# Performance work log

Hardware: AMD Instinct MI355X
Metric: run time of the kernel (lower is better)

The kernel has to match this reference:

```python
import jax, jax.numpy as jnp
import numpy as np

B, N, C, C_OUT, LAYERS, ORDER = 512, 207, 207, 512, 2, 2
EPS = 1e-5


def setup_inputs() -> dict:
    key = jax.random.key(0)
    ks = jax.random.split(key, 12)
    C3 = (ORDER * 1 + 1) * C  # support_len=1 (adaptive only), order=2 -> 3*C
    inp = {
        "x": jax.random.normal(ks[0], (B, N, C), dtype=jnp.float32),
        "nodevec1": jax.random.normal(ks[1], (N, 10), dtype=jnp.float32),
        "nodevec2": jax.random.normal(ks[2], (10, N), dtype=jnp.float32),
        # per-layer gcn 1x1 conv: (layers, C_out=C, C_in=3C) + bias
        "Wg": jax.random.normal(ks[3], (LAYERS, C, C3), dtype=jnp.float32) * (1.0 / np.sqrt(C3)),
        "bg": jax.random.normal(ks[4], (LAYERS, C), dtype=jnp.float32) * 0.01,
        # per-layer BatchNorm1d (eval mode) params over channel dim C
        "gamma": 1.0 + 0.1 * jax.random.normal(ks[5], (LAYERS, C), dtype=jnp.float32),
        "beta": 0.1 * jax.random.normal(ks[6], (LAYERS, C), dtype=jnp.float32),
        "rmean": 0.1 * jax.random.normal(ks[7], (LAYERS, C), dtype=jnp.float32),
        "rvar": jax.random.uniform(ks[8], (LAYERS, C), dtype=jnp.float32, minval=0.5, maxval=1.5),
        # final Conv1d(C, C_OUT, k=1)
        "Wm": jax.random.normal(ks[9], (C_OUT, C), dtype=jnp.float32) * (1.0 / np.sqrt(C)),
        "bm": jax.random.normal(ks[10], (C_OUT,), dtype=jnp.float32) * 0.01,
    }
    return inp


def reference(x, nodevec1, nodevec2, Wg, bg, gamma, beta, rmean, rvar, Wm, bm):
    # x: (B, N, C) -> (B, C, N)
    h = jnp.transpose(x, (0, 2, 1))
    # adaptive adjacency: softmax(relu(E1 @ E2), axis=1), shape (N, N)
    adp = jax.nn.softmax(jax.nn.relu(nodevec1 @ nodevec2), axis=1)
    for i in range(LAYERS):
        # diffusion conv: out[b,c,w] = sum_v h[b,c,v] * A[w,v]  (einsum 'ncvl,nwv->ncwl')
        x1 = jnp.einsum('bcv,wv->bcw', h, adp)
        x2 = jnp.einsum('bcv,wv->bcw', x1, adp)
        cat = jnp.concatenate([h, x1, x2], axis=1)  # (B, 3C, N)
        # 1x1 conv (linear over channels) + bias
        g = jnp.einsum('bcn,oc->bon', cat, Wg[i]) + bg[i][None, :, None]
        # BatchNorm1d in eval mode (dropout is identity at inference)
        inv = gamma[i] / jnp.sqrt(rvar[i] + EPS)
        h = g * inv[None, :, None] + (beta[i] - rmean[i] * inv)[None, :, None]
    # final Conv1d 1x1: C -> C_OUT
    out = jnp.einsum('bcn,oc->bon', h, Wm) + bm[None, :, None]  # (B, C_OUT, N)
    return jnp.transpose(out, (0, 2, 1))  # (B, N, C_OUT)
```

## Files before the change

kernel.cpp:

```cpp
#include <hip/hip_runtime.h>
#include <hip/hip_bf16.h>

#define B 512
#define N 207
#define C 207
#define CO 512
#define NLAYERS 2
#define EPS 1e-5f

#define STRIDE 224
#define ROWS 208
#define KSTEPS 7
#define RS ((size_t)ROWS*STRIDE)
#define XSTR 232

typedef unsigned short ushort;
typedef short s8v __attribute__((ext_vector_type(8)));
typedef float f4 __attribute__((ext_vector_type(4)));
typedef unsigned short u16x4 __attribute__((ext_vector_type(4)));

__device__ __forceinline__ ushort f2bu(float f) {
    __hip_bfloat16 h = __float2bfloat16(f);
    return __builtin_bit_cast(ushort, h);
}
__device__ __forceinline__ float bu2f(ushort u) {
    union { unsigned int u; float f; } v; v.u = ((unsigned int)u) << 16;
    return v.f;
}
__device__ __forceinline__ u16x4 packbf4(f4 v) {
    u16x4 r;
    #pragma unroll
    for (int i = 0; i < 4; ++i) r[i] = f2bu(v[i]);
    return r;
}

__global__ void adp_kernel(const float* __restrict__ nv1, const float* __restrict__ nv2,
                           ushort* __restrict__ P1) {
    int w = blockIdx.x, j = threadIdx.x;
    __shared__ float red[256];
    if (w >= 207) {
        if (j < STRIDE) P1[w*STRIDE + j] = 0;
        return;
    }
    float val = 0.f;
    if (j < 207) {
        float acc = 0.f;
        #pragma unroll
        for (int k = 0; k < 10; ++k) acc += nv1[w*10 + k] * nv2[k*207 + j];
        val = fmaxf(acc, 0.f);
    }
    red[j] = (j < 207) ? val : -1e30f;
    __syncthreads();
    for (int off = 128; off > 0; off >>= 1) {
        if (j < off) red[j] = fmaxf(red[j], red[j+off]);
        __syncthreads();
    }
    float m = red[0];
    __syncthreads();
    float e = (j < 207) ? expf(val - m) : 0.f;
    red[j] = e;
    __syncthreads();
    for (int off = 128; off > 0; off >>= 1) {
        if (j < off) red[j] += red[j+off];
        __syncthreads();
    }
    float inv = 1.f / red[0];
    if (j < STRIDE) P1[w*STRIDE + j] = f2bu(e * inv);
}

__global__ void p2_kernel(const ushort* __restrict__ P1, ushort* __restrict__ P2) {
    int v = blockIdx.x*16 + threadIdx.x;
    int w = blockIdx.y*16 + threadIdx.y;
    if (w < STRIDE && v < STRIDE) {
        float acc = 0.f;
        for (int u = 0; u < 207; ++u) acc += bu2f(P1[w*STRIDE + u]) * bu2f(P1[u*STRIDE + v]);
        P2[w*STRIDE + v] = f2bu(acc);
    }
}

__global__ void bn_kernel(const float* __restrict__ gamma, const float* __restrict__ beta,
                          const float* __restrict__ rmean, const float* __restrict__ rvar,
                          const float* __restrict__ bg,
                          float* __restrict__ binv, float* __restrict__ bfold) {
    int i = blockIdx.x*256 + threadIdx.x;
    if (i >= NLAYERS*ROWS) return;
    int l = i / ROWS, o = i % ROWS;
    float iv = 0.f, bf = 0.f;
    if (o < 207) {
        float g = gamma[l*207 + o];
        iv = g * rsqrtf(rvar[l*207 + o] + EPS);
        bf = bg[l*207 + o]*iv + beta[l*207 + o] - rmean[l*207 + o]*iv;
    }
    binv[i] = iv; bfold[i] = bf;
}

__global__ void wg_prep(const float* __restrict__ Wg, ushort* __restrict__ Wgp) {
    int idx = blockIdx.x*256 + threadIdx.x;
    if (idx >= NLAYERS*3*ROWS*STRIDE) return;
    int k = idx % STRIDE;
    int o = (idx / STRIDE) % ROWS;
    int seg = (idx / (STRIDE*ROWS)) % 3;
    int l = idx / (STRIDE*ROWS*3);
    float v = (o < 207 && k < 207) ? Wg[((size_t)(l*207 + o))*621 + seg*207 + k] : 0.f;
    Wgp[idx] = f2bu(v);
}

__global__ void wm_prep(const float* __restrict__ Wm, ushort* __restrict__ Wmp) {
    int idx = blockIdx.x*256 + threadIdx.x;
    if (idx >= CO*STRIDE) return;
    int k = idx % STRIDE, o = idx / STRIDE;
    Wmp[idx] = f2bu(k < 207 ? Wm[o*207 + k] : 0.f);
}

__global__ void h0_kernel(const float* __restrict__ x, ushort* __restrict__ Hcv,
                          ushort* __restrict__ Hnc) {
    __shared__ float t[32][33];
    int b = blockIdx.z;
    int n0 = blockIdx.x*32, c0 = blockIdx.y*32;
    int tx = threadIdx.x, ty = threadIdx.y;
    for (int i = ty; i < 32; i += 8) {
        int n = n0 + i, c = c0 + tx;
        t[i][tx] = (n < 207 && c < 207) ? x[((size_t)b*207 + n)*207 + c] : 0.f;
    }
    __syncthreads();
    size_t base = (size_t)b*RS;
    for (int i = ty; i < 32; i += 8) {
        int n = n0 + i, c = c0 + tx;
        if (n < ROWS && c < STRIDE) Hnc[base + (size_t)n*STRIDE + c] = f2bu(t[i][tx]);
    }
    for (int i = ty; i < 32; i += 8) {
        int c = c0 + i, n = n0 + tx;
        if (c < ROWS && n < STRIDE) Hcv[base + (size_t)c*STRIDE + n] = f2bu(t[tx][i]);
    }
}

template<int ROUNDS_>
__device__ __forceinline__ void stage512(ushort* __restrict__ tile,
                                         const ushort* __restrict__ src,
                                         int rbase, int rmax, int kbase, int tid) {
    int lane = tid & 63, wave = tid >> 6;
    #pragma unroll
    for (int i = 0; i < ROUNDS_; ++i) {
        int r = rbase + i*128 + wave*16 + (lane >> 2);
        r = (r > rmax) ? rmax : r;
        const ushort* g = src + (size_t)r*STRIDE + kbase + (lane & 3)*8;
        ushort* l = tile + i*4096 + wave*512;
        __builtin_amdgcn_global_load_lds(
            (const __attribute__((address_space(1))) void*)g,
            (__attribute__((address_space(3))) void*)l, 16, 0, 0);
    }
}

#define WAIT_VM(n) asm volatile("s_waitcnt vmcnt(" #n ")" ::: "memory")
#define WAIT_LGKM0 asm volatile("s_waitcnt lgkmcnt(0)" ::: "memory")

__global__ __launch_bounds__(512, 2)
void layer_kernel(const ushort* __restrict__ Hcv, const ushort* __restrict__ Hnc,
                  const ushort* __restrict__ P1, const ushort* __restrict__ P2,
                  const ushort* __restrict__ Wgl,
                  const float* __restrict__ bi, const float* __restrict__ bsh,
                  ushort* __restrict__ Hcv_out, ushort* __restrict__ Hnc_out) {
    __shared__ __align__(16) ushort lds[75776];
    ushort* A1t = lds;
    ushort* A2t = lds + 12288;
    ushort* Bt  = lds + 24576;
    ushort* Wgt = lds + 59392;
    ushort* X1l = lds;
    ushort* X2l = lds + 29696;
    ushort* Hnct = lds;

    int tile = blockIdx.x;
    int b = blockIdx.y;
    int n0 = tile*128;
    size_t boff = (size_t)b*RS;
    const ushort* Hcvb = Hcv + boff;
    const ushort* Hncb = Hnc + boff;

    int tid = threadIdx.x, lane = tid & 63, wid = tid >> 6;
    int frow = lane & 15, fko = (lane >> 4)*8, g4 = (lane >> 4)*4;

    int wmA = wid >> 1, wnA = wid & 1;
    f4 aX1[2][8], aX2[2][8];
    #pragma unroll
    for (int i = 0; i < 2; ++i)
        #pragma unroll
        for (int j = 0; j < 8; ++j) { aX1[i][j] = (f4)0.f; aX2[i][j] = (f4)0.f; }

    #pragma unroll
    for (int t = 0; t < 2; ++t) {
        stage512<1>(A1t + t*4096, P1, n0, 223, t*32, tid);
        stage512<1>(A2t + t*4096, P2, n0, 223, t*32, tid);
        stage512<2>(Bt  + t*8192, Hcvb, 0, 207, t*32, tid);
    }

    for (int ks = 0; ks < KSTEPS; ++ks) {
        int bi3 = ks % 3;
        if (ks <= 4) {
            int t = ks + 2, b3 = t % 3;
            stage512<1>(A1t + b3*4096, P1, n0, 223, t*32, tid);
            stage512<1>(A2t + b3*4096, P2, n0, 223, t*32, tid);
            stage512<2>(Bt  + b3*8192, Hcvb, 0, 207, t*32, tid);
            WAIT_VM(8);
        } else if (ks == 5) {
            stage512<2>(Wgt, Wgl + RS, 0, 207, 0, tid);
            WAIT_VM(6);
        } else {
            WAIT_VM(2);
        }
        __builtin_amdgcn_s_barrier();
        s8v a1[2], a2[2], bfr[8];
        #pragma unroll
        for (int f = 0; f < 2; ++f) {
            a1[f] = *(const s8v*)&A1t[bi3*4096 + (wmA*32 + f*16 + frow)*32 + fko];
            a2[f] = *(const s8v*)&A2t[bi3*4096 + (wmA*32 + f*16 + frow)*32 + fko];
        }
        #pragma unroll
        for (int f = 0; f < 8; ++f)
            bfr[f] = *(const s8v*)&Bt[bi3*8192 + (wnA*128 + f*16 + frow)*32 + fko];
        #pragma unroll
        for (int fm = 0; fm < 2; ++fm)
            #pragma unroll
            for (int fn = 0; fn < 8; ++fn) {
                aX1[fm][fn] = __builtin_amdgcn_mfma_f32_16x16x32_bf16(bfr[fn], a1[fm], aX1[fm][fn], 0, 0, 0);
                aX2[fm][fn] = __builtin_amdgcn_mfma_f32_16x16x32_bf16(bfr[fn], a2[fm], aX2[fm][fn], 0, 0, 0);
            }
        WAIT_LGKM0;
        __builtin_amdgcn_s_barrier();
    }
    #pragma unroll
    for (int fm = 0; fm < 2; ++fm) {
        int w = wmA*32 + fm*16 + (lane & 15);
        #pragma unroll
        for (int fn = 0; fn < 8; ++fn) {
            int cq = wnA*128 + fn*16 + g4;
            if (cq < STRIDE) {
                *(u16x4*)&X1l[w*XSTR + cq] = packbf4(aX1[fm][fn]);
                *(u16x4*)&X2l[w*XSTR + cq] = packbf4(aX2[fm][fn]);
            }
        }
    }
    WAIT_LGKM0;
    __builtin_amdgcn_s_barrier();

    int wmB = wid >> 1, wnB = wid & 1;
    f4 aG[4][4];
    #pragma unroll
    for (int i = 0; i < 4; ++i)
        #pragma unroll
        for (int j = 0; j < 4; ++j) aG[i][j] = (f4)0.f;

    const int NK = 3*KSTEPS;
    for (int ks = 0; ks < NK; ++ks) {
        int cur = ks & 1;
        int seg = (ks < 7) ? 1 : (ks < 14) ? 2 : 0;
        int k0 = (ks % 7)*32;
        if (ks + 1 < NK) {
            int ks1 = ks + 1;
            int seg1v = (ks1 < 7) ? 1 : (ks1 < 14) ? 2 : 0;
            int kk1 = (ks1 % 7)*32;
            stage512<2>(Wgt + (cur^1)*8192, Wgl + (size_t)seg1v*RS, 0, 207, kk1, tid);
        }
        if (ks >= 7 && ks <= 13) {
            stage512<1>(Hnct + (ks-7)*4096, Hncb, n0, 207, (ks-7)*32, tid);
        }
        if (ks == NK-1) { WAIT_VM(0); }
        else if (ks >= 7 && ks <= 13) { WAIT_VM(3); }
        else { WAIT_VM(2); }
        __builtin_amdgcn_s_barrier();
        s8v a[4], bfr[4];
        #pragma unroll
        for (int f = 0; f < 4; ++f)
            a[f] = *(const s8v*)&Wgt[cur*8192 + (wmB*64 + f*16 + frow)*32 + fko];
        if (seg == 0) {
            const ushort* ht = Hnct + (ks - 14)*4096;
            #pragma unroll
            for (int fn = 0; fn < 4; ++fn)
                bfr[fn] = *(const s8v*)&ht[(wnB*64 + fn*16 + frow)*32 + fko];
        } else {
            const ushort* Xs = (seg == 1) ? X1l : X2l;
            #pragma unroll
            for (int fn = 0; fn < 4; ++fn) {
                int row = wnB*64 + fn*16 + frow;
                bfr[fn] = *(const s8v*)&Xs[row*XSTR + k0 + fko];
            }
        }
        #pragma unroll
        for (int fm = 0; fm < 4; ++fm)
            #pragma unroll
            for (int fn = 0; fn < 4; ++fn)
                aG[fm][fn] = __builtin_amdgcn_mfma_f32_16x16x32_bf16(bfr[fn], a[fm], aG[fm][fn], 0, 0, 0);
        WAIT_LGKM0;
        __builtin_amdgcn_s_barrier();
    }

    ushort* Ocv = Hcv_out + boff;
    ushort* Onc = Hnc_out + boff;
    #pragma unroll
    for (int fm = 0; fm < 4; ++fm) {
        int o = wmB*64 + fm*16 + (lane & 15);
        if (o >= ROWS) continue;
        float iv = bi[o], sh = bsh[o];
        #pragma unroll
        for (int fn = 0; fn < 4; ++fn) {
            int nq = n0 + wnB*64 + fn*16 + g4;
            if (nq >= STRIDE) continue;
            f4 h = aG[fm][fn]*iv + sh;
            u16x4 hq = packbf4(h);
            *(u16x4*)(Ocv + (size_t)o*STRIDE + nq) = hq;
            #pragma unroll
            for (int r = 0; r < 4; ++r) {
                int n = nq + r;
                if (n < ROWS) Onc[(size_t)n*STRIDE + o] = hq[r];
            }
        }
    }
}

__global__ __launch_bounds__(512, 2)
void final_kernel(const ushort* __restrict__ Hnc, const ushort* __restrict__ Wmp,
                  const float* __restrict__ bm, float* __restrict__ out) {
    __shared__ __align__(16) ushort At[2][128*32], Bt[2][512*32];
    int b = blockIdx.y;
    int n0 = blockIdx.x*128;
    const ushort* Hb = Hnc + (size_t)b*RS;
    int tid = threadIdx.x, lane = tid & 63, wid = tid >> 6;
    int wo = wid >> 1, wn = wid & 1;
    int frow = lane & 15, fko = (lane >> 4)*8;

    f4 acc[4][8];
    #pragma unroll
    for (int i = 0; i < 4; ++i)
        #pragma unroll
        for (int j = 0; j < 8; ++j) acc[i][j] = (f4)0.f;

    stage512<1>(At[0], Hb,  n0, 207, 0, tid);
    stage512<4>(Bt[0], Wmp, 0, 511, 0, tid);

    for (int ks = 0; ks < KSTEPS; ++ks) {
        int cur = ks & 1;
        if (ks + 1 < KSTEPS) {
            int k1 = (ks + 1)*32;
            stage512<1>(At[cur^1], Hb,  n0, 207, k1, tid);
            stage512<4>(Bt[cur^1], Wmp, 0, 511, k1, tid);
            WAIT_VM(5);
        } else {
            WAIT_VM(0);
        }
        __builtin_amdgcn_s_barrier();
        s8v a[4], bf[8];
        #pragma unroll
        for (int f = 0; f < 4; ++f)
            a[f]  = *(const s8v*)&At[cur][(wn*64 + f*16 + frow)*32 + fko];
        #pragma unroll
        for (int f = 0; f < 8; ++f)
            bf[f] = *(const s8v*)&Bt[cur][(wo*128 + f*16 + frow)*32 + fko];
        #pragma unroll
        for (int fm = 0; fm < 4; ++fm)
            #pragma unroll
            for (int fn = 0; fn < 8; ++fn)
                acc[fm][fn] = __builtin_amdgcn_mfma_f32_16x16x32_bf16(bf[fn], a[fm], acc[fm][fn], 0, 0, 0);
        WAIT_LGKM0;
        __builtin_amdgcn_s_barrier();
    }

    int g4 = (lane >> 4)*4;
    #pragma unroll
    for (int fm = 0; fm < 4; ++fm) {
        int n = n0 + wn*64 + fm*16 + (lane & 15);
        if (n >= 207) continue;
        float* orow = out + ((size_t)b*207 + n)*CO;
        #pragma unroll
        for (int fn = 0; fn < 8; ++fn) {
            int oq = wo*128 + fn*16 + g4;
            f4 bias = *(const f4*)(bm + oq);
            f4 v = acc[fm][fn] + bias;
            *(f4*)(orow + oq) = v;
        }
    }
}

static inline size_t align_up(size_t v, size_t a) { return (v + a - 1) & ~(a - 1); }

extern "C" void kernel_launch(void* const* d_in, const int* in_sizes, int n_in,
                              void* d_out, int out_size, void* d_ws, size_t ws_size,
                              hipStream_t stream) {
    const float* x     = (const float*)d_in[0];
    const float* nv1   = (const float*)d_in[1];
    const float* nv2   = (const float*)d_in[2];
    const float* Wg    = (const float*)d_in[3];
    const float* bg    = (const float*)d_in[4];
    const float* gamma = (const float*)d_in[5];
    const float* beta  = (const float*)d_in[6];
    const float* rmean = (const float*)d_in[7];
    const float* rvar  = (const float*)d_in[8];
    const float* Wm    = (const float*)d_in[9];
    const float* bm    = (const float*)d_in[10];
    float* out = (float*)d_out;

    char* ws = (char*)d_ws;
    const size_t bufN = (size_t)B*RS*sizeof(ushort);
    ushort* P1   = (ushort*)ws; ws += align_up((size_t)STRIDE*STRIDE*2, 512);
    ushort* P2   = (ushort*)ws; ws += align_up((size_t)STRIDE*STRIDE*2, 512);
    float* binv  = (float*)ws;  ws += align_up((size_t)NLAYERS*ROWS*4, 512);
    float* bfold = (float*)ws;  ws += align_up((size_t)NLAYERS*ROWS*4, 512);
    ushort* Wgp  = (ushort*)ws; ws += align_up((size_t)NLAYERS*3*RS*2, 512);
    ushort* Wmp  = (ushort*)ws; ws += align_up((size_t)CO*STRIDE*2, 512);
    ushort* A0 = (ushort*)ws; ws += align_up(bufN, 512);
    ushort* A1 = (ushort*)ws; ws += align_up(bufN, 512);
    ushort* B0 = (ushort*)ws; ws += align_up(bufN, 512);
    ushort* B1 = (ushort*)ws; ws += align_up(bufN, 512);

    adp_kernel<<<STRIDE, 256, 0, stream>>>(nv1, nv2, P1);
    p2_kernel<<<dim3(14, 14), dim3(16, 16), 0, stream>>>(P1, P2);
    bn_kernel<<<(NLAYERS*ROWS + 255)/256, 256, 0, stream>>>(gamma, beta, rmean, rvar, bg, binv, bfold);
    wg_prep<<<(NLAYERS*3*ROWS*STRIDE + 255)/256, 256, 0, stream>>>(Wg, Wgp);
    wm_prep<<<(CO*STRIDE + 255)/256, 256, 0, stream>>>(Wm, Wmp);
    h0_kernel<<<dim3(7, 7, B), dim3(32, 8), 0, stream>>>(x, A0, A1);

    layer_kernel<<<dim3(2, B), 512, 0, stream>>>(A0, A1, P1, P2,
        Wgp, binv, bfold, B0, B1);
    layer_kernel<<<dim3(2, B), 512, 0, stream>>>(B0, B1, P1, P2,
        Wgp + (size_t)3*RS, binv + ROWS, bfold + ROWS, A0, A1);

    final_kernel<<<dim3(2, B), 512, 0, stream>>>(A1, Wmp, bm, out);
}
```

Measured before the change: 385.8 us.

## Swizzle LDS tiles, double-buffer diffusion loads, stream Wg/H directly into registers

Applies an XOR swizzle to the 16-byte chunk placement in LDS staging and to the matching MFMA fragment reads, to cut bank conflicts in both the layer and final kernels. Reduces the diffusion stage from triple to double buffering. The 1x1-conv stage now loads Wg and H tiles straight from global memory into registers with double-buffered inline-asm loads, with no LDS staging and no per-step barriers. This lowers LDS use, which may raise occupancy, but costs more VGPRs, and each wave now does redundant global loads instead of sharing them through LDS.

```diff
diff --git a/kernel.cpp b/kernel.cpp
--- a/kernel.cpp
+++ b/kernel.cpp
@@ -33,6 +33,16 @@
     for (int i = 0; i < 4; ++i) r[i] = f2bu(v[i]);
     return r;
 }
+
+__device__ __forceinline__ s8v gload16(const ushort* p) {
+    s8v v;
+    asm volatile("global_load_dwordx4 %0, %1, off"
+                 : "=v"(v) : "v"(p) : "memory");
+    return v;
+}
+
+#define WAIT_VM(n) asm volatile("s_waitcnt vmcnt(" #n ")" ::: "memory")
+#define WAIT_LGKM0 asm volatile("s_waitcnt lgkmcnt(0)" ::: "memory")
 
 __global__ void adp_kernel(const float* __restrict__ nv1, const float* __restrict__ nv2,
                            ushort* __restrict__ P1) {
@@ -139,20 +149,18 @@
                                          const ushort* __restrict__ src,
                                          int rbase, int rmax, int kbase, int tid) {
     int lane = tid & 63, wave = tid >> 6;
+    int chunk = ((lane & 3) ^ ((lane >> 3) & 3)) * 8;
     #pragma unroll
     for (int i = 0; i < ROUNDS_; ++i) {
         int r = rbase + i*128 + wave*16 + (lane >> 2);
         r = (r > rmax) ? rmax : r;
-        const ushort* g = src + (size_t)r*STRIDE + kbase + (lane & 3)*8;
+        const ushort* g = src + (size_t)r*STRIDE + kbase + chunk;
         ushort* l = tile + i*4096 + wave*512;
         __builtin_amdgcn_global_load_lds(
             (const __attribute__((address_space(1))) void*)g,
             (__attribute__((address_space(3))) void*)l, 16, 0, 0);
     }
 }
-
-#define WAIT_VM(n) asm volatile("s_waitcnt vmcnt(" #n ")" ::: "memory")
-#define WAIT_LGKM0 asm volatile("s_waitcnt lgkmcnt(0)" ::: "memory")
 
 __global__ __launch_bounds__(512, 2)
 void layer_kernel(const ushort* __restrict__ Hcv, const ushort* __restrict__ Hnc,
@@ -160,14 +168,12 @@
                   const ushort* __restrict__ Wgl,
                   const float* __restrict__ bi, const float* __restrict__ bsh,
                   ushort* __restrict__ Hcv_out, ushort* __restrict__ Hnc_out) {
-    __shared__ __align__(16) ushort lds[75776];
+    __shared__ __align__(16) ushort lds[59392];
     ushort* A1t = lds;
-    ushort* A2t = lds + 12288;
-    ushort* Bt  = lds + 24576;
-    ushort* Wgt = lds + 59392;
+    ushort* A2t = lds + 8192;
+    ushort* Bt  = lds + 16384;
     ushort* X1l = lds;
     ushort* X2l = lds + 29696;
-    ushort* Hnct = lds;
 
     int tile = blockIdx.x;
     int b = blockIdx.y;
@@ -177,7 +183,10 @@
     const ushort* Hncb = Hnc + boff;
 
     int tid = threadIdx.x, lane = tid & 63, wid = tid >> 6;
-    int frow = lane & 15, fko = (lane >> 4)*8, g4 = (lane >> 4)*4;
+    int frow = lane & 15;
+    int fko   = (lane >> 4)*8;
+    int fko_s = (((lane >> 4) ^ ((lane >> 1) & 3)))*8;
+    int g4 = (lane >> 4)*4;
 
     int wmA = wid >> 1, wnA = wid & 1;
     f4 aX1[2][8], aX2[2][8];
@@ -186,37 +195,31 @@
         #pragma unroll
         for (int j = 0; j < 8; ++j) { aX1[i][j] = (f4)0.f; aX2[i][j] = (f4)0.f; }
 
-    #pragma unroll
-    for (int t = 0; t < 2; ++t) {
-        stage512<1>(A1t + t*4096, P1, n0, 223, t*32, tid);
-        stage512<1>(A2t + t*4096, P2, n0, 223, t*32, tid);
-        stage512<2>(Bt  + t*8192, Hcvb, 0, 207, t*32, tid);
-    }
+    stage512<1>(A1t, P1, n0, 223, 0, tid);
+    stage512<1>(A2t, P2, n0, 223, 0, tid);
+    stage512<2>(Bt,  Hcvb, 0, 207, 0, tid);
 
     for (int ks = 0; ks < KSTEPS; ++ks) {
-        int bi3 = ks % 3;
-        if (ks <= 4) {
-            int t = ks + 2, b3 = t % 3;
-            stage512<1>(A1t + b3*4096, P1, n0, 223, t*32, tid);
-            stage512<1>(A2t + b3*4096, P2, n0, 223, t*32, tid);
-            stage512<2>(Bt  + b3*8192, Hcvb, 0, 207, t*32, tid);
-            WAIT_VM(8);
-        } else if (ks == 5) {
-            stage512<2>(Wgt, Wgl + RS, 0, 207, 0, tid);
-            WAIT_VM(6);
+        int cur = ks & 1;
+        if (ks + 1 < KSTEPS) {
+            int k1 = (ks + 1)*32;
+            stage512<1>(A1t + (cur^1)*4096, P1, n0, 223, k1, tid);
+            stage512<1>(A2t + (cur^1)*4096, P2, n0, 223, k1, tid);
+            stage512<2>(Bt  + (cur^1)*8192, Hcvb, 0, 207, k1, tid);
+            WAIT_VM(4);
         } else {
-            WAIT_VM(2);
+            WAIT_VM(0);
         }
         __builtin_amdgcn_s_barrier();
         s8v a1[2], a2[2], bfr[8];
         #pragma unroll
         for (int f = 0; f < 2; ++f) {
-            a1[f] = *(const s8v*)&A1t[bi3*4096 + (wmA*32 + f*16 + frow)*32 + fko];
-            a2[f] = *(const s8v*)&A2t[bi3*4096 + (wmA*32 + f*16 + frow)*32 + fko];
+            a1[f] = *(const s8v*)&A1t[cur*4096 + (wmA*32 + f*16 + frow)*32 + fko_s];
+            a2[f] = *(const s8v*)&A2t[cur*4096 + (wmA*32 + f*16 + frow)*32 + fko_s];
         }
         #pragma unroll
         for (int f = 0; f < 8; ++f)
-            bfr[f] = *(const s8v*)&Bt[bi3*8192 + (wnA*128 + f*16 + frow)*32 + fko];
+            bfr[f] = *(const s8v*)&Bt[cur*8192 + (wnA*128 + f*16 + frow)*32 + fko_s];
         #pragma unroll
         for (int fm = 0; fm < 2; ++fm)
             #pragma unroll
@@ -249,48 +252,63 @@
         #pragma unroll
         for (int j = 0; j < 4; ++j) aG[i][j] = (f4)0.f;
 
-    const int NK = 3*KSTEPS;
-    for (int ks = 0; ks < NK; ++ks) {
-        int cur = ks & 1;
-        int seg = (ks < 7) ? 1 : (ks < 14) ? 2 : 0;
-        int k0 = (ks % 7)*32;
-        if (ks + 1 < NK) {
-            int ks1 = ks + 1;
-            int seg1v = (ks1 < 7) ? 1 : (ks1 < 14) ? 2 : 0;
-            int kk1 = (ks1 % 7)*32;
-            stage512<2>(Wgt + (cur^1)*8192, Wgl + (size_t)seg1v*RS, 0, 207, kk1, tid);
-        }
-        if (ks >= 7 && ks <= 13) {
-            stage512<1>(Hnct + (ks-7)*4096, Hncb, n0, 207, (ks-7)*32, tid);
-        }
-        if (ks == NK-1) { WAIT_VM(0); }
-        else if (ks >= 7 && ks <= 13) { WAIT_VM(3); }
-        else { WAIT_VM(2); }
-        __builtin_amdgcn_s_barrier();
-        s8v a[4], bfr[4];
-        #pragma unroll
-        for (int f = 0; f < 4; ++f)
-            a[f] = *(const s8v*)&Wgt[cur*8192 + (wmB*64 + f*16 + frow)*32 + fko];
+    const ushort* wseg[3] = { Wgl, Wgl + RS, Wgl + 2*RS };
+    size_t woff[4];
+    #pragma unroll
+    for (int f = 0; f < 4; ++f) {
+        int o = wmB*64 + f*16 + frow;
+        if (o > 207) o = 207;
+        woff[f] = (size_t)o*STRIDE + fko;
+    }
+    const ushort* hptr[4];
+    #pragma unroll
+    for (int f = 0; f < 4; ++f) {
+        int n = n0 + wnB*64 + f*16 + frow;
+        if (n > 207) n = 207;
+        hptr[f] = Hncb + (size_t)n*STRIDE + fko;
+    }
+
+    s8v wbuf[2][4], hbuf[2][4];
+    #pragma unroll
+    for (int f = 0; f < 4; ++f)
+        wbuf[0][f] = gload16(wseg[1] + woff[f]);
+
+    #pragma unroll
+    for (int ks = 0; ks < 21; ++ks) {
+        const int seg = (ks < 7) ? 1 : (ks < 14) ? 2 : 0;
+        const int k0  = (ks % 7)*32;
+        if (ks + 1 < 21) {
+            const int seg1 = (ks+1 < 7) ? 1 : (ks+1 < 14) ? 2 : 0;
+            const int k01  = ((ks+1) % 7)*32;
+            #pragma unroll
+            for (int f = 0; f < 4; ++f)
+                wbuf[(ks+1)&1][f] = gload16(wseg[seg1] + woff[f] + k01);
+            if (seg1 == 0) {
+                #pragma unroll
+                for (int f = 0; f < 4; ++f)
+                    hbuf[(ks+1)&1][f] = gload16(hptr[f] + k01);
+            }
+        }
+        if (ks == 20)      { WAIT_VM(0); }
+        else if (ks >= 13) { WAIT_VM(8); }
+        else               { WAIT_VM(4); }
+        __builtin_amdgcn_sched_barrier(0);
+
+        s8v bfr[4];
         if (seg == 0) {
-            const ushort* ht = Hnct + (ks - 14)*4096;
-            #pragma unroll
-            for (int fn = 0; fn < 4; ++fn)
-                bfr[fn] = *(const s8v*)&ht[(wnB*64 + fn*16 + frow)*32 + fko];
+            #pragma unroll
+            for (int fn = 0; fn < 4; ++fn) bfr[fn] = hbuf[ks&1][fn];
         } else {
             const ushort* Xs = (seg == 1) ? X1l : X2l;
             #pragma unroll
-            for (int fn = 0; fn < 4; ++fn) {
-                int row = wnB*64 + fn*16 + frow;
-                bfr[fn] = *(const s8v*)&Xs[row*XSTR + k0 + fko];
-            }
+            for (int fn = 0; fn < 4; ++fn)
+                bfr[fn] = *(const s8v*)&Xs[(wnB*64 + fn*16 + frow)*XSTR + k0 + fko];
         }
         #pragma unroll
         for (int fm = 0; fm < 4; ++fm)
             #pragma unroll
             for (int fn = 0; fn < 4; ++fn)
-                aG[fm][fn] = __builtin_amdgcn_mfma_f32_16x16x32_bf16(bfr[fn], a[fm], aG[fm][fn], 0, 0, 0);
-        WAIT_LGKM0;
-        __builtin_amdgcn_s_barrier();
+                aG[fm][fn] = __builtin_amdgcn_mfma_f32_16x16x32_bf16(bfr[fn], wbuf[ks&1][fm], aG[fm][fn], 0, 0, 0);
     }
 
     ushort* Ocv = Hcv_out + boff;
@@ -325,7 +343,8 @@
     const ushort* Hb = Hnc + (size_t)b*RS;
     int tid = threadIdx.x, lane = tid & 63, wid = tid >> 6;
     int wo = wid >> 1, wn = wid & 1;
-    int frow = lane & 15, fko = (lane >> 4)*8;
+    int frow = lane & 15;
+    int fko_s = (((lane >> 4) ^ ((lane >> 1) & 3)))*8;
 
     f4 acc[4][8];
     #pragma unroll
@@ -350,10 +369,10 @@
         s8v a[4], bf[8];
         #pragma unroll
         for (int f = 0; f < 4; ++f)
-            a[f]  = *(const s8v*)&At[cur][(wn*64 + f*16 + frow)*32 + fko];
+            a[f]  = *(const s8v*)&At[cur][(wn*64 + f*16 + frow)*32 + fko_s];
         #pragma unroll
         for (int f = 0; f < 8; ++f)
-            bf[f] = *(const s8v*)&Bt[cur][(wo*128 + f*16 + frow)*32 + fko];
+            bf[f] = *(const s8v*)&Bt[cur][(wo*128 + f*16 + frow)*32 + fko_s];
         #pragma unroll
         for (int fm = 0; fm < 4; ++fm)
             #pragma unroll
```

After: 391.6 us. No clear change (+1.5%).
